# Performance work log

Measured on AMD Instinct MI355X. Metric: run time of the kernel, lower is better.

Reference implementation:

```python
import jax, jax.numpy as jnp
import numpy as np

INF = 1e10
NX = 1024
N_HEAD = 16
HEAD_DIM = NX // N_HEAD
N_CTX = 1024
B = 4
T = 1024
REL_VOCAB = 64


def setup_inputs() -> dict:
    key = jax.random.key(0)
    ks = jax.random.split(key, 9)
    s = 0.02
    return {
        "x": jax.random.normal(ks[0], (B, T, NX), jnp.float32),
        "rel": jax.random.randint(ks[1], (B, T, T), 0, REL_VOCAB),
        "w_attn": jax.random.normal(ks[2], (NX, 3 * NX), jnp.float32) * s,
        "b_attn": jnp.zeros((3 * NX,), jnp.float32),
        "w_proj": jax.random.normal(ks[3], (NX, NX), jnp.float32) * s,
        "b_proj": jnp.zeros((NX,), jnp.float32),
        "rel_weights": jax.random.normal(ks[4], (REL_VOCAB, N_HEAD), jnp.float32) * s,
        "rel_values": jax.random.normal(ks[5], (REL_VOCAB, HEAD_DIM), jnp.float32) * s,
        "rel_ids": jax.random.randint(ks[6], (N_CTX, N_CTX), 0, REL_VOCAB),
    }


def reference(x, rel, w_attn, b_attn, w_proj, b_proj, rel_weights, rel_values, rel_ids):
    b, t, _ = x.shape
    qkv = x @ w_attn + b_attn                      # [B,T,3*NX]
    q, k, v = jnp.split(qkv, 3, axis=-1)
    split = lambda z: z.reshape(b, t, N_HEAD, HEAD_DIM).transpose(0, 2, 1, 3)
    q, k, v = split(q), split(k), split(v)         # [B,H,T,D]

    w = jnp.einsum('bhtd,bhsd->bhts', q, k) / jnp.sqrt(jnp.float32(HEAD_DIM))

    bias = jnp.tril(jnp.ones((t, t), jnp.float32))  # causal mask [T,T]
    rel_b = rel_weights[rel].transpose(0, 3, 1, 2)  # [B,H,T,T] (use_tree)

    # additive relative bias, then causal mask with -INF fill
    w = w + rel_b * bias
    w = w * bias - INF * (1.0 - bias)
    p = jax.nn.softmax(w, axis=-1)                  # [B,H,T,T]

    ret = jnp.einsum('bhts,bhsd->bhtd', p, v)

    # use_seq: relative-value contribution
    rel_v = rel_values[rel_ids[:t, :t]]             # [T,T,D]
    ret = ret + jnp.einsum('bhts,tsd->bhtd', p, rel_v)

    a = ret.transpose(0, 2, 1, 3).reshape(b, t, NX)  # merge heads
    return a @ w_proj + b_proj
```

## Files before the change

### kernel.cpp

```cpp
#include <hip/hip_runtime.h>
#include <hip/hip_bf16.h>

typedef __bf16 bf16;
typedef __bf16 bf16x8 __attribute__((ext_vector_type(8)));
typedef float f32x4 __attribute__((ext_vector_type(4)));
typedef unsigned char u8;
typedef unsigned int u32;
typedef unsigned short u16;
typedef u16 ushort4v __attribute__((ext_vector_type(4)));
typedef u32 u32x4 __attribute__((ext_vector_type(4)));

#define B_ 4
#define T_ 1024
#define NX_ 1024
#define NH_ 16
#define HD_ 64

__device__ __forceinline__ void gld16(const void* g, void* l) {
  __builtin_amdgcn_global_load_lds((const __attribute__((address_space(1))) void*)g,
                                   (__attribute__((address_space(3))) void*)l, 16, 0, 0);
}

__global__ __launch_bounds__(256) void k_cvt(const float* __restrict__ in, bf16* __restrict__ out, int n) {
  int i = (blockIdx.x * 256 + threadIdx.x) * 4;
  if (i + 3 < n) {
    float4 v = *(const float4*)(in + i);
    out[i] = (bf16)v.x; out[i + 1] = (bf16)v.y; out[i + 2] = (bf16)v.z; out[i + 3] = (bf16)v.w;
  }
}

__global__ __launch_bounds__(256) void k_transpose(const float* __restrict__ in, bf16* __restrict__ out, int K, int N) {
  __shared__ float tile[64][65];
  int n0 = blockIdx.x * 64, k0 = blockIdx.y * 64;
  for (int i = threadIdx.x; i < 4096; i += 256) {
    int r = i >> 6, c = i & 63;
    tile[r][c] = in[(size_t)(k0 + r) * N + n0 + c];
  }
  __syncthreads();
  for (int i = threadIdx.x; i < 4096; i += 256) {
    int r = i >> 6, c = i & 63;
    out[(size_t)(n0 + r) * K + k0 + c] = (bf16)tile[c][r];
  }
}

__global__ __launch_bounds__(256) void k_pack(const int* __restrict__ rel, const int* __restrict__ rel_ids,
                                              u8* __restrict__ dst8) {
  int i = (blockIdx.x * 256 + threadIdx.x) * 4;
  const int* src = (i < 4194304) ? (rel + i) : (rel_ids + (i - 4194304));
  int4 v = *(const int4*)src;
  uchar4 o = {(u8)v.x, (u8)v.y, (u8)v.z, (u8)v.w};
  *(uchar4*)(dst8 + i) = o;
}

__global__ __launch_bounds__(256) void k_rvt(const float* __restrict__ rel_values, bf16* __restrict__ rvT) {
  int d = threadIdx.x >> 2, seg = threadIdx.x & 3;
  for (int i = 0; i < 16; ++i) {
    int rr = seg * 16 + i;
    rvT[d * 64 + rr] = (bf16)rel_values[rr * 64 + d];
  }
}

template <int EPI>
__global__ __launch_bounds__(256) void k_gemm(
    const bf16* __restrict__ A, const bf16* __restrict__ BT, const float* __restrict__ bias,
    float* __restrict__ outF, bf16* __restrict__ qg, bf16* __restrict__ kg, bf16* __restrict__ vtg,
    int M, int N, int K) {
  __shared__ __align__(16) bf16 Ab[2][128 * 32];
  __shared__ __align__(16) bf16 Bb[2][128 * 32];
  int tid = threadIdx.x, lane = tid & 63, w = tid >> 6;
  int wm = w >> 1, wn = w & 1;
  int m0 = blockIdx.y * 128, n0 = blockIdx.x * 128;
  int sl = lane >> 4, lr = lane & 15;
  f32x4 acc[4][4] = {};
  int NKt = K >> 5;

  auto stage = [&](int kt, int bidx) {
    const bf16* Ag = A + (size_t)m0 * K + kt * 32;
    const bf16* Bg = BT + (size_t)n0 * K + kt * 32;
#pragma unroll
    for (int j = 0; j < 2; ++j) {
      int c = w * 128 + j * 64 + lane;
      int row = c >> 2, slot = c & 3;
      int ss = slot ^ ((row >> 1) & 3);
      gld16(Ag + (size_t)row * K + ss * 8, &Ab[bidx][(w * 128 + j * 64) * 8]);
      gld16(Bg + (size_t)row * K + ss * 8, &Bb[bidx][(w * 128 + j * 64) * 8]);
    }
  };
  stage(0, 0);
  for (int kt = 0; kt < NKt; ++kt) {
    int bidx = kt & 1;
    __syncthreads();
    if (kt + 1 < NKt) stage(kt + 1, bidx ^ 1);
    bf16x8 af[4], bfv[4];
#pragma unroll
    for (int mi = 0; mi < 4; ++mi) {
      int row = wm * 64 + mi * 16 + lr;
      af[mi] = *(const bf16x8*)&Ab[bidx][row * 32 + ((sl ^ ((row >> 1) & 3)) * 8)];
    }
#pragma unroll
    for (int ni = 0; ni < 4; ++ni) {
      int row = wn * 64 + ni * 16 + lr;
      bfv[ni] = *(const bf16x8*)&Bb[bidx][row * 32 + ((sl ^ ((row >> 1) & 3)) * 8)];
    }
#pragma unroll
    for (int mi = 0; mi < 4; ++mi)
#pragma unroll
      for (int ni = 0; ni < 4; ++ni)
        acc[mi][ni] = __builtin_amdgcn_mfma_f32_16x16x32_bf16(af[mi], bfv[ni], acc[mi][ni], 0, 0, 0);
  }
#pragma unroll
  for (int ni = 0; ni < 4; ++ni) {
    int n = n0 + wn * 64 + ni * 16 + lr;
    float bv = bias[n];
#pragma unroll
    for (int mi = 0; mi < 4; ++mi) {
      int mb = m0 + wm * 64 + mi * 16 + sl * 4;
#pragma unroll
      for (int r = 0; r < 4; ++r) {
        float v = acc[mi][ni][r] + bv;
        int m = mb + r;
        if (EPI == 0) {
          int region = n >> 10, hh = (n & 1023) >> 6, d = n & 63;
          int bb = m >> 10, t = m & 1023;
          int bh = bb * NH_ + hh;
          if (region == 0)      qg[((size_t)bh * T_ + t) * HD_ + d] = (bf16)v;
          else if (region == 1) kg[((size_t)bh * T_ + t) * HD_ + d] = (bf16)v;
          else                  vtg[((size_t)bh * HD_ + d) * T_ + t] = (bf16)v;
        } else {
          outF[(size_t)m * N + n] = v;
        }
      }
    }
  }
}


#define GLD4(dst, ptr) asm volatile("global_load_dwordx4 %0, %1, off" : "=v"(dst) : "v"(ptr))
#define GLD1(dst, ptr) asm volatile("global_load_dword %0, %1, off" : "=v"(dst) : "v"(ptr))

#define LOADKV(s0v, k00, k01, k10, k11, v0, v1, v2, v3, rid0, rid1, iid0, iid1)  \
  do {                                                                           \
    int s0_ = (s0v);                                                             \
    GLD4(k00, klane + (size_t)s0_ * HD_);                                        \
    GLD4(k01, klane + (size_t)s0_ * HD_ + 32);                                   \
    GLD4(k10, klane + (size_t)(s0_ + 16) * HD_);                                 \
    GLD4(k11, klane + (size_t)(s0_ + 16) * HD_ + 32);                            \
    GLD4(v0, vlane + s0_);                                                       \
    GLD4(v1, vlane + 16 * T_ + s0_);                                             \
    GLD4(v2, vlane + 32 * T_ + s0_);                                             \
    GLD4(v3, vlane + 48 * T_ + s0_);                                             \
    GLD1(rid0, ridlane + s0_);                                                   \
    GLD1(rid1, ridlane + s0_ + 16);                                              \
    GLD1(iid0, iidlane + s0_);                                                   \
    GLD1(iid1, iidlane + s0_ + 16);                                              \
  } while (0)

#define COMPUTE(s0v, k00, k01, k10, k11, v0, v1, v2, v3, rid0, rid1, iid0, iid1) \
  do {                                                                           \
    int s0_ = (s0v);                                                             \
    bf16x8 qf0_ = __builtin_bit_cast(bf16x8, qr0);                               \
    bf16x8 qf1_ = __builtin_bit_cast(bf16x8, qr1);                               \
    f32x4 S0_ = {}, S1_ = {};                                                    \
    S0_ = __builtin_amdgcn_mfma_f32_16x16x32_bf16(__builtin_bit_cast(bf16x8, k00), qf0_, S0_, 0, 0, 0); \
    S0_ = __builtin_amdgcn_mfma_f32_16x16x32_bf16(__builtin_bit_cast(bf16x8, k01), qf1_, S0_, 0, 0, 0); \
    S1_ = __builtin_amdgcn_mfma_f32_16x16x32_bf16(__builtin_bit_cast(bf16x8, k10), qf0_, S1_, 0, 0, 0); \
    S1_ = __builtin_amdgcn_mfma_f32_16x16x32_bf16(__builtin_bit_cast(bf16x8, k11), qf1_, S1_, 0, 0, 0); \
    u16 pb_[8];                                                                  \
    {                                                                            \
      int sbase_ = s0_ + sl * 4;                                                 \
      _Pragma("unroll") for (int r = 0; r < 4; ++r) {                            \
        float e = (sbase_ + r <= tglob)                                          \
                      ? __expf(S0_[r] * 0.125f) * tab[(rid0 >> (8 * r)) & 63]    \
                      : 0.f;                                                     \
        lsum += e;                                                               \
        bf16 eb = (bf16)e;                                                       \
        pb_[r] = *(u16*)&eb;                                                     \
        if (e != 0.f) atomicAdd(&prel[lr * 68 + ((iid0 >> (8 * r)) & 63)], e);   \
      }                                                                          \
      sbase_ += 16;                                                              \
      _Pragma("unroll") for (int r = 0; r < 4; ++r) {                            \
        float e = (sbase_ + r <= tglob)                                          \
                      ? __expf(S1_[r] * 0.125f) * tab[(rid1 >> (8 * r)) & 63]    \
                      : 0.f;                                                     \
        lsum += e;                                                               \
        bf16 eb = (bf16)e;                                                       \
        pb_[4 + r] = *(u16*)&eb;                                                 \
        if (e != 0.f) atomicAdd(&prel[lr * 68 + ((iid1 >> (8 * r)) & 63)], e);   \
      }                                                                          \
    }                                                                            \
    u32 a0_ = (u32)pb_[0] | ((u32)pb_[1] << 16);                                 \
    u32 b0_ = (u32)pb_[2] | ((u32)pb_[3] << 16);                                 \
    u32 a1_ = (u32)pb_[4] | ((u32)pb_[5] << 16);                                 \
    u32 b1_ = (u32)pb_[6] | ((u32)pb_[7] << 16);                                 \
    int srcA_ = lr + (((sl & 1) * 2) << 4);                                      \
    int srcB_ = srcA_ + 16;                                                      \
    u32 taA0_ = (u32)__shfl((int)a0_, srcA_), taA1_ = (u32)__shfl((int)a1_, srcA_); \
    u32 tbA0_ = (u32)__shfl((int)b0_, srcA_), tbA1_ = (u32)__shfl((int)b1_, srcA_); \
    u32 taB0_ = (u32)__shfl((int)a0_, srcB_), taB1_ = (u32)__shfl((int)a1_, srcB_); \
    u32 tbB0_ = (u32)__shfl((int)b0_, srcB_), tbB1_ = (u32)__shfl((int)b1_, srcB_); \
    bool hi_ = (sl & 2) != 0;                                                    \
    u32x4 wv_;                                                                   \
    wv_[0] = hi_ ? taA1_ : taA0_;                                                \
    wv_[1] = hi_ ? tbA1_ : tbA0_;                                                \
    wv_[2] = hi_ ? taB1_ : taB0_;                                                \
    wv_[3] = hi_ ? tbB1_ : tbB0_;                                                \
    bf16x8 pfrag_ = __builtin_bit_cast(bf16x8, wv_);                             \
    acc[0] = __builtin_amdgcn_mfma_f32_16x16x32_bf16(__builtin_bit_cast(bf16x8, v0), pfrag_, acc[0], 0, 0, 0); \
    acc[1] = __builtin_amdgcn_mfma_f32_16x16x32_bf16(__builtin_bit_cast(bf16x8, v1), pfrag_, acc[1], 0, 0, 0); \
    acc[2] = __builtin_amdgcn_mfma_f32_16x16x32_bf16(__builtin_bit_cast(bf16x8, v2), pfrag_, acc[2], 0, 0, 0); \
    acc[3] = __builtin_amdgcn_mfma_f32_16x16x32_bf16(__builtin_bit_cast(bf16x8, v3), pfrag_, acc[3], 0, 0, 0); \
  } while (0)

#define WAIT12() do { asm volatile("s_waitcnt vmcnt(12)" ::: "memory"); __builtin_amdgcn_sched_barrier(0); } while (0)
#define WAIT0()  do { asm volatile("s_waitcnt vmcnt(0)"  ::: "memory"); __builtin_amdgcn_sched_barrier(0); } while (0)

__global__ __launch_bounds__(256, 2) void k_attn(
    const bf16* __restrict__ qg, const bf16* __restrict__ kg, const bf16* __restrict__ vtg,
    const u8* __restrict__ rel8, const float* __restrict__ rel_weights,
    const u8* __restrict__ relid8, const bf16* __restrict__ rvT,
    bf16* __restrict__ ret) {
  __shared__ float prelBase[4 * 1088];
  __shared__ float tabBase[4 * 64];

  int bid = blockIdx.x;
  int x = bid & 7, j = bid >> 3;
  int b = x >> 1;
  int h = (x & 1) + ((j >> 3) << 1);
  int q = j & 7;
  int w = threadIdx.x >> 6;
  int lane = threadIdx.x & 63;
  int lr = lane & 15, sl = lane >> 4;
  int p = q * 4 + w;
  int bh = b * NH_ + h;

  float* prel = prelBase + w * 1088;
  float* tab = tabBase + w * 64;
  tab[lane] = __expf(rel_weights[lane * NH_ + h]);

  const u8* relbase = rel8 + (size_t)b * T_ * T_;

#pragma unroll
  for (int side = 0; side < 2; ++side) {
    int tt = side ? p : 63 - p;
    int t0 = tt * 16;
    int tglob = t0 + lr;

#pragma unroll
    for (int i = 0; i < 17; ++i) prel[i * 64 + lane] = 0.f;

    const bf16* qrow = qg + ((size_t)bh * T_ + t0 + lr) * HD_;
    const bf16* klane = kg + ((size_t)bh * T_ + lr) * HD_ + sl * 8;
    const bf16* vlane = vtg + ((size_t)bh * HD_ + lr) * T_ + sl * 8;
    const u8* ridlane = relbase + (size_t)(t0 + lr) * T_ + sl * 4;
    const u8* iidlane = relid8 + (size_t)(t0 + lr) * T_ + sl * 4;

    f32x4 acc[4] = {};
    float lsum = 0.f;

    u32x4 qr0, qr1;
    GLD4(qr0, qrow + sl * 8);
    GLD4(qr1, qrow + 32 + sl * 8);

    u32x4 ak00, ak01, ak10, ak11, av0, av1, av2, av3;
    u32 arid0, arid1, aiid0, aiid1;
    u32x4 bk00, bk01, bk10, bk11, bv0, bv1, bv2, bv3;
    u32 brid0, brid1, biid0, biid1;

    int nst = (tt >> 1) + 1;
    LOADKV(0, ak00, ak01, ak10, ak11, av0, av1, av2, av3, arid0, arid1, aiid0, aiid1);
    for (int st = 0; st < nst; st += 2) {
      if (st + 1 < nst) {
        LOADKV((st + 1) * 32, bk00, bk01, bk10, bk11, bv0, bv1, bv2, bv3, brid0, brid1, biid0, biid1);
        WAIT12();
      } else {
        WAIT0();
      }
      COMPUTE(st * 32, ak00, ak01, ak10, ak11, av0, av1, av2, av3, arid0, arid1, aiid0, aiid1);
      if (st + 1 < nst) {
        if (st + 2 < nst) {
          LOADKV((st + 2) * 32, ak00, ak01, ak10, ak11, av0, av1, av2, av3, arid0, arid1, aiid0, aiid1);
          WAIT12();
        } else {
          WAIT0();
        }
        COMPUTE((st + 1) * 32, bk00, bk01, bk10, bk11, bv0, bv1, bv2, bv3, brid0, brid1, biid0, biid1);
      }
    }

    float v = lsum;
    v += __shfl_xor(v, 16);
    v += __shfl_xor(v, 32);
    float inv = 1.f / v;

    asm volatile("s_waitcnt lgkmcnt(0)" ::: "memory");
    __builtin_amdgcn_sched_barrier(0);
#pragma unroll
    for (int kc = 0; kc < 2; ++kc) {
      f32x4 pA = *(const f32x4*)&prel[lr * 68 + kc * 32 + sl * 8];
      f32x4 pB = *(const f32x4*)&prel[lr * 68 + kc * 32 + sl * 8 + 4];
      u16 pb[8];
#pragma unroll
      for (int jj = 0; jj < 4; ++jj) { bf16 xx = (bf16)pA[jj]; pb[jj] = *(u16*)&xx; }
#pragma unroll
      for (int jj = 0; jj < 4; ++jj) { bf16 xx = (bf16)pB[jj]; pb[4 + jj] = *(u16*)&xx; }
      bf16x8 pfrag = *(bf16x8*)&pb[0];
#pragma unroll
      for (int ni = 0; ni < 4; ++ni) {
        bf16x8 af = *(const bf16x8*)(rvT + (size_t)(ni * 16 + lr) * 64 + kc * 32 + sl * 8);
        acc[ni] = __builtin_amdgcn_mfma_f32_16x16x32_bf16(af, pfrag, acc[ni], 0, 0, 0);
      }
    }

    bf16* rp = ret + ((size_t)(b * T_ + t0 + lr)) * NX_ + h * HD_ + sl * 4;
#pragma unroll
    for (int ni = 0; ni < 4; ++ni) {
      ushort4v ov;
#pragma unroll
      for (int r = 0; r < 4; ++r) {
        bf16 xx = (bf16)(acc[ni][r] * inv);
        ov[r] = *(u16*)&xx;
      }
      *(ushort4v*)(rp + ni * 16) = ov;
    }
    asm volatile("s_waitcnt lgkmcnt(0)" ::: "memory");
  }
}

extern "C" void kernel_launch(void* const* d_in, const int* in_sizes, int n_in,
                              void* d_out, int out_size, void* d_ws, size_t ws_size,
                              hipStream_t stream) {
  const float* x = (const float*)d_in[0];
  const int* rel = (const int*)d_in[1];
  const float* w_attn = (const float*)d_in[2];
  const float* b_attn = (const float*)d_in[3];
  const float* w_proj = (const float*)d_in[4];
  const float* b_proj = (const float*)d_in[5];
  const float* rel_weights = (const float*)d_in[6];
  const float* rel_values = (const float*)d_in[7];
  const int* rel_ids = (const int*)d_in[8];
  float* out = (float*)d_out;

  char* ws = (char*)d_ws;
  bf16* xb  = (bf16*)(ws);
  bf16* wTa = (bf16*)(ws + 8388608);
  bf16* wTp = (bf16*)(ws + 14680064);
  bf16* qg  = (bf16*)(ws + 16777216);
  bf16* kg  = (bf16*)(ws + 25165824);
  bf16* vtg = (bf16*)(ws + 33554432);
  bf16* ret = (bf16*)(ws + 41943040);
  u8* rel8   = (u8*)(ws);
  u8* relid8 = (u8*)(ws + 4194304);
  bf16* rvT  = (bf16*)(ws + 5242880);

  k_cvt<<<4096, 256, 0, stream>>>(x, xb, 4194304);
  k_transpose<<<dim3(48, 16), 256, 0, stream>>>(w_attn, wTa, 1024, 3072);
  k_transpose<<<dim3(16, 16), 256, 0, stream>>>(w_proj, wTp, 1024, 1024);
  k_gemm<0><<<dim3(24, 32), 256, 0, stream>>>(xb, wTa, b_attn, nullptr, qg, kg, vtg, 4096, 3072, 1024);
  k_pack<<<5120, 256, 0, stream>>>(rel, rel_ids, rel8);
  k_rvt<<<1, 256, 0, stream>>>(rel_values, rvT);
  k_attn<<<512, 256, 0, stream>>>(qg, kg, vtg, rel8, rel_weights, relid8, rvT, ret);
  k_gemm<1><<<dim3(8, 32), 256, 0, stream>>>(ret, wTp, b_proj, out, nullptr, nullptr, nullptr, 4096, 1024, 1024);
}
```

Baseline: 272.7 us.

## Split attention key range across four waves with LDS partial-sum reduction

Each 16-row query tile is now handled by a whole block, and its four waves interleave over the key chunks (split-K), instead of one wave walking all key chunks. Partial PV accumulators are stored as bf16 in LDS with row sums, then one wave reduces them, applies the rel-value MFMA and writes out. The grid grows from 512 to 2048 blocks and occupancy is raised to 3 blocks per CU, to fix load imbalance and the long serial loop per wave. In exchange it adds block barriers, an LDS reduction pass, and some precision loss from storing partial sums in bf16.

```diff
diff --git a/kernel.cpp b/kernel.cpp
--- a/kernel.cpp
+++ b/kernel.cpp
@@ -135,8 +135,8 @@
 }
 
 
-#define GLD4(dst, ptr) asm volatile("global_load_dwordx4 %0, %1, off" : "=v"(dst) : "v"(ptr))
-#define GLD1(dst, ptr) asm volatile("global_load_dword %0, %1, off" : "=v"(dst) : "v"(ptr))
+#define GLD4(dst, ptr) asm volatile("global_load_dwordx4 %0, %1, off" : "=&v"(dst) : "v"(ptr))
+#define GLD1(dst, ptr) asm volatile("global_load_dword %0, %1, off" : "=&v"(dst) : "v"(ptr))
 
 #define LOADKV(s0v, k00, k01, k10, k11, v0, v1, v2, v3, rid0, rid1, iid0, iid1)  \
   do {                                                                           \
@@ -214,116 +214,140 @@
 #define WAIT12() do { asm volatile("s_waitcnt vmcnt(12)" ::: "memory"); __builtin_amdgcn_sched_barrier(0); } while (0)
 #define WAIT0()  do { asm volatile("s_waitcnt vmcnt(0)"  ::: "memory"); __builtin_amdgcn_sched_barrier(0); } while (0)
 
-__global__ __launch_bounds__(256, 2) void k_attn(
+#define DO_PHASE(TTv, PRELP)                                                     \
+  {                                                                              \
+    int tt = (TTv);                                                              \
+    int t0 = tt * 16;                                                            \
+    int tglob = t0 + lr;                                                         \
+    float* prel = (PRELP);                                                       \
+    const bf16* qrow = qg + ((size_t)bh * T_ + t0 + lr) * HD_;                   \
+    const bf16* klane = kg + ((size_t)bh * T_ + lr) * HD_ + sl * 8;              \
+    const bf16* vlane = vtg + ((size_t)bh * HD_ + lr) * T_ + sl * 8;             \
+    const u8* ridlane = relbase + (size_t)(t0 + lr) * T_ + sl * 4;               \
+    const u8* iidlane = relid8 + (size_t)(t0 + lr) * T_ + sl * 4;                \
+    int nst = (tt >> 1) + 1;                                                     \
+    lsum = 0.f;                                                                  \
+    acc[0] = f32x4{0.f, 0.f, 0.f, 0.f}; acc[1] = f32x4{0.f, 0.f, 0.f, 0.f};      \
+    acc[2] = f32x4{0.f, 0.f, 0.f, 0.f}; acc[3] = f32x4{0.f, 0.f, 0.f, 0.f};      \
+    if (wv < nst) {                                                              \
+      u32x4 qr0, qr1;                                                            \
+      GLD4(qr0, qrow + sl * 8);                                                  \
+      GLD4(qr1, qrow + 32 + sl * 8);                                             \
+      u32x4 ak00, ak01, ak10, ak11, av0, av1, av2, av3;                          \
+      u32 arid0, arid1, aiid0, aiid1;                                            \
+      u32x4 bk00, bk01, bk10, bk11, bv0, bv1, bv2, bv3;                          \
+      u32 brid0, brid1, biid0, biid1;                                            \
+      LOADKV(wv * 32, ak00, ak01, ak10, ak11, av0, av1, av2, av3, arid0, arid1, aiid0, aiid1); \
+      for (int st = wv; st < nst; st += 8) {                                     \
+        if (st + 4 < nst) {                                                      \
+          LOADKV((st + 4) * 32, bk00, bk01, bk10, bk11, bv0, bv1, bv2, bv3, brid0, brid1, biid0, biid1); \
+          WAIT12();                                                              \
+        } else {                                                                 \
+          WAIT0();                                                               \
+        }                                                                        \
+        COMPUTE(st * 32, ak00, ak01, ak10, ak11, av0, av1, av2, av3, arid0, arid1, aiid0, aiid1); \
+        if (st + 4 < nst) {                                                      \
+          if (st + 8 < nst) {                                                    \
+            LOADKV((st + 8) * 32, ak00, ak01, ak10, ak11, av0, av1, av2, av3, arid0, arid1, aiid0, aiid1); \
+            WAIT12();                                                            \
+          } else {                                                               \
+            WAIT0();                                                             \
+          }                                                                      \
+          COMPUTE((st + 4) * 32, bk00, bk01, bk10, bk11, bv0, bv1, bv2, bv3, brid0, brid1, biid0, biid1); \
+        }                                                                        \
+      }                                                                          \
+    }                                                                            \
+    u32* obw = (u32*)obuf + ((wv << 6) + lane) * 9;                              \
+    _Pragma("unroll") for (int ni = 0; ni < 4; ++ni) {                           \
+      bf16 e0 = (bf16)acc[ni][0], e1 = (bf16)acc[ni][1];                         \
+      bf16 e2 = (bf16)acc[ni][2], e3 = (bf16)acc[ni][3];                         \
+      obw[ni * 2 + 0] = (u32)*(u16*)&e0 | ((u32)*(u16*)&e1 << 16);               \
+      obw[ni * 2 + 1] = (u32)*(u16*)&e2 | ((u32)*(u16*)&e3 << 16);               \
+    }                                                                            \
+    lsbuf[(wv << 6) + lane] = lsum;                                              \
+  }
+
+#define DO_EPI(TTv, PRELP)                                                       \
+  {                                                                              \
+    int tt = (TTv);                                                              \
+    int t0 = tt * 16;                                                            \
+    float* prel = (PRELP);                                                       \
+    float ls = lsbuf[lane] + lsbuf[64 + lane] + lsbuf[128 + lane] + lsbuf[192 + lane]; \
+    ls += __shfl_xor(ls, 16);                                                    \
+    ls += __shfl_xor(ls, 32);                                                    \
+    float inv = 1.f / ls;                                                        \
+    f32x4 eacc[4] = {};                                                          \
+    _Pragma("unroll") for (int wp = 0; wp < 4; ++wp) {                           \
+      const u32* obr = (const u32*)obuf + ((wp << 6) + lane) * 9;                \
+      _Pragma("unroll") for (int ni = 0; ni < 4; ++ni) {                         \
+        u32 v0 = obr[ni * 2], v1 = obr[ni * 2 + 1];                              \
+        u16 tu0 = (u16)v0, tu1 = (u16)(v0 >> 16), tu2 = (u16)v1, tu3 = (u16)(v1 >> 16); \
+        eacc[ni][0] += (float)*(bf16*)&tu0;                                      \
+        eacc[ni][1] += (float)*(bf16*)&tu1;                                      \
+        eacc[ni][2] += (float)*(bf16*)&tu2;                                      \
+        eacc[ni][3] += (float)*(bf16*)&tu3;                                      \
+      }                                                                          \
+    }                                                                            \
+    _Pragma("unroll") for (int kc = 0; kc < 2; ++kc) {                           \
+      f32x4 pA = *(const f32x4*)&prel[lr * 68 + kc * 32 + sl * 8];               \
+      f32x4 pB = *(const f32x4*)&prel[lr * 68 + kc * 32 + sl * 8 + 4];           \
+      u16 pb[8];                                                                 \
+      _Pragma("unroll") for (int jj = 0; jj < 4; ++jj) { bf16 xx = (bf16)pA[jj]; pb[jj] = *(u16*)&xx; } \
+      _Pragma("unroll") for (int jj = 0; jj < 4; ++jj) { bf16 xx = (bf16)pB[jj]; pb[4 + jj] = *(u16*)&xx; } \
+      bf16x8 pfrag = *(bf16x8*)&pb[0];                                           \
+      _Pragma("unroll") for (int ni = 0; ni < 4; ++ni) {                         \
+        bf16x8 af = *(const bf16x8*)(rvT + (size_t)(ni * 16 + lr) * 64 + kc * 32 + sl * 8); \
+        eacc[ni] = __builtin_amdgcn_mfma_f32_16x16x32_bf16(af, pfrag, eacc[ni], 0, 0, 0); \
+      }                                                                          \
+    }                                                                            \
+    bf16* rp = ret + ((size_t)(b * T_ + t0 + lr)) * NX_ + h * HD_ + sl * 4;      \
+    _Pragma("unroll") for (int ni = 0; ni < 4; ++ni) {                           \
+      ushort4v ov;                                                               \
+      _Pragma("unroll") for (int r = 0; r < 4; ++r) {                            \
+        bf16 xx = (bf16)(eacc[ni][r] * inv);                                     \
+        ov[r] = *(u16*)&xx;                                                      \
+      }                                                                          \
+      *(ushort4v*)(rp + ni * 16) = ov;                                           \
+    }                                                                            \
+  }
+
+__global__ __launch_bounds__(256, 3) void k_attn(
     const bf16* __restrict__ qg, const bf16* __restrict__ kg, const bf16* __restrict__ vtg,
     const u8* __restrict__ rel8, const float* __restrict__ rel_weights,
     const u8* __restrict__ relid8, const bf16* __restrict__ rvT,
     bf16* __restrict__ ret) {
-  __shared__ float prelBase[4 * 1088];
-  __shared__ float tabBase[4 * 64];
+  __shared__ float prelH[1088];
+  __shared__ float prelL[1088];
+  __shared__ float tab[64];
+  __shared__ float lsbuf[256];
+  __shared__ __align__(16) u16 obuf[4608];
 
   int bid = blockIdx.x;
   int x = bid & 7, j = bid >> 3;
   int b = x >> 1;
-  int h = (x & 1) + ((j >> 3) << 1);
-  int q = j & 7;
-  int w = threadIdx.x >> 6;
+  int h = (x & 1) + ((j >> 5) << 1);
+  int p = j & 31;
+  int wv = threadIdx.x >> 6;
   int lane = threadIdx.x & 63;
   int lr = lane & 15, sl = lane >> 4;
-  int p = q * 4 + w;
   int bh = b * NH_ + h;
 
-  float* prel = prelBase + w * 1088;
-  float* tab = tabBase + w * 64;
-  tab[lane] = __expf(rel_weights[lane * NH_ + h]);
+  if (threadIdx.x < 64) tab[threadIdx.x] = __expf(rel_weights[threadIdx.x * NH_ + h]);
+  for (int i = threadIdx.x; i < 1088; i += 256) { prelH[i] = 0.f; prelL[i] = 0.f; }
+  __syncthreads();
 
   const u8* relbase = rel8 + (size_t)b * T_ * T_;
 
-#pragma unroll
-  for (int side = 0; side < 2; ++side) {
-    int tt = side ? p : 63 - p;
-    int t0 = tt * 16;
-    int tglob = t0 + lr;
-
-#pragma unroll
-    for (int i = 0; i < 17; ++i) prel[i * 64 + lane] = 0.f;
-
-    const bf16* qrow = qg + ((size_t)bh * T_ + t0 + lr) * HD_;
-    const bf16* klane = kg + ((size_t)bh * T_ + lr) * HD_ + sl * 8;
-    const bf16* vlane = vtg + ((size_t)bh * HD_ + lr) * T_ + sl * 8;
-    const u8* ridlane = relbase + (size_t)(t0 + lr) * T_ + sl * 4;
-    const u8* iidlane = relid8 + (size_t)(t0 + lr) * T_ + sl * 4;
-
-    f32x4 acc[4] = {};
-    float lsum = 0.f;
-
-    u32x4 qr0, qr1;
-    GLD4(qr0, qrow + sl * 8);
-    GLD4(qr1, qrow + 32 + sl * 8);
-
-    u32x4 ak00, ak01, ak10, ak11, av0, av1, av2, av3;
-    u32 arid0, arid1, aiid0, aiid1;
-    u32x4 bk00, bk01, bk10, bk11, bv0, bv1, bv2, bv3;
-    u32 brid0, brid1, biid0, biid1;
-
-    int nst = (tt >> 1) + 1;
-    LOADKV(0, ak00, ak01, ak10, ak11, av0, av1, av2, av3, arid0, arid1, aiid0, aiid1);
-    for (int st = 0; st < nst; st += 2) {
-      if (st + 1 < nst) {
-        LOADKV((st + 1) * 32, bk00, bk01, bk10, bk11, bv0, bv1, bv2, bv3, brid0, brid1, biid0, biid1);
-        WAIT12();
-      } else {
-        WAIT0();
-      }
-      COMPUTE(st * 32, ak00, ak01, ak10, ak11, av0, av1, av2, av3, arid0, arid1, aiid0, aiid1);
-      if (st + 1 < nst) {
-        if (st + 2 < nst) {
-          LOADKV((st + 2) * 32, ak00, ak01, ak10, ak11, av0, av1, av2, av3, arid0, arid1, aiid0, aiid1);
-          WAIT12();
-        } else {
-          WAIT0();
-        }
-        COMPUTE((st + 1) * 32, bk00, bk01, bk10, bk11, bv0, bv1, bv2, bv3, brid0, brid1, biid0, biid1);
-      }
-    }
-
-    float v = lsum;
-    v += __shfl_xor(v, 16);
-    v += __shfl_xor(v, 32);
-    float inv = 1.f / v;
-
-    asm volatile("s_waitcnt lgkmcnt(0)" ::: "memory");
-    __builtin_amdgcn_sched_barrier(0);
-#pragma unroll
-    for (int kc = 0; kc < 2; ++kc) {
-      f32x4 pA = *(const f32x4*)&prel[lr * 68 + kc * 32 + sl * 8];
-      f32x4 pB = *(const f32x4*)&prel[lr * 68 + kc * 32 + sl * 8 + 4];
-      u16 pb[8];
-#pragma unroll
-      for (int jj = 0; jj < 4; ++jj) { bf16 xx = (bf16)pA[jj]; pb[jj] = *(u16*)&xx; }
-#pragma unroll
-      for (int jj = 0; jj < 4; ++jj) { bf16 xx = (bf16)pB[jj]; pb[4 + jj] = *(u16*)&xx; }
-      bf16x8 pfrag = *(bf16x8*)&pb[0];
-#pragma unroll
-      for (int ni = 0; ni < 4; ++ni) {
-        bf16x8 af = *(const bf16x8*)(rvT + (size_t)(ni * 16 + lr) * 64 + kc * 32 + sl * 8);
-        acc[ni] = __builtin_amdgcn_mfma_f32_16x16x32_bf16(af, pfrag, acc[ni], 0, 0, 0);
-      }
-    }
-
-    bf16* rp = ret + ((size_t)(b * T_ + t0 + lr)) * NX_ + h * HD_ + sl * 4;
-#pragma unroll
-    for (int ni = 0; ni < 4; ++ni) {
-      ushort4v ov;
-#pragma unroll
-      for (int r = 0; r < 4; ++r) {
-        bf16 xx = (bf16)(acc[ni][r] * inv);
-        ov[r] = *(u16*)&xx;
-      }
-      *(ushort4v*)(rp + ni * 16) = ov;
-    }
-    asm volatile("s_waitcnt lgkmcnt(0)" ::: "memory");
-  }
+  f32x4 acc[4];
+  float lsum;
+
+  DO_PHASE(63 - p, prelH);
+  __syncthreads();
+  if (wv == 0) DO_EPI(63 - p, prelH);
+  __syncthreads();
+  DO_PHASE(p, prelL);
+  __syncthreads();
+  if (wv == 1) DO_EPI(p, prelL);
 }
 
 extern "C" void kernel_launch(void* const* d_in, const int* in_sizes, int n_in,
@@ -358,6 +382,6 @@
   k_gemm<0><<<dim3(24, 32), 256, 0, stream>>>(xb, wTa, b_attn, nullptr, qg, kg, vtg, 4096, 3072, 1024);
   k_pack<<<5120, 256, 0, stream>>>(rel, rel_ids, rel8);
   k_rvt<<<1, 256, 0, stream>>>(rel_values, rvT);
-  k_attn<<<512, 256, 0, stream>>>(qg, kg, vtg, rel8, rel_weights, relid8, rvT, ret);
+  k_attn<<<2048, 256, 0, stream>>>(qg, kg, vtg, rel8, rel_weights, relid8, rvT, ret);
   k_gemm<1><<<dim3(8, 32), 256, 0, stream>>>(ret, wTp, b_proj, out, nullptr, nullptr, nullptr, 4096, 1024, 1024);
 }
```

New measurement: 287.2 us. 5.3% more time.
